# Optimization experiments

Measured on AMD Instinct MI355X. Metric: run time of the kernel, lower is better.

The kernel has to match this reference:

```python
import jax, jax.numpy as jnp
import numpy as np

EPS = 1e-8

def setup_inputs() -> dict:
    key = jax.random.key(0)
    ks = jax.random.split(key, 7)
    B, S, H, NH, V = 4, 2048, 1024, 8, 2048
    sc = 1.0 / np.sqrt(H)
    return {
        "hidden": jax.random.normal(ks[0], (B, S, H), jnp.float32),
        "prior_w": jax.random.normal(ks[1], (H, NH), jnp.float32) * sc,
        "prior_b": jnp.zeros((NH,), jnp.float32),
        "latent_w": jax.random.normal(ks[2], (H, NH * H), jnp.float32) * sc,
        "latent_b": jnp.zeros((NH * H,), jnp.float32),
        "output_w": jax.random.normal(ks[3], (H, V), jnp.float32) * sc,
        "output_b": jnp.zeros((V,), jnp.float32),
    }

def reference(hidden, prior_w, prior_b, latent_w, latent_b, output_w, output_b):
    B, S, H = hidden.shape
    NH = prior_w.shape[1]
    # prior: sigmoid then renormalize over heads
    prior = jax.nn.sigmoid(hidden @ prior_w + prior_b)              # [B,S,NH]
    prior = prior / (prior.sum(-1, keepdims=True) + EPS)
    # latent: linear -> [B,S,NH,H] -> tanh
    latent = jnp.tanh((hidden @ latent_w + latent_b).reshape(B, S, NH, H))
    # per-head softmax over vocab, weighted sum over heads
    logits = jnp.einsum('bsnh,hv->bsnv', latent, output_w) + output_b
    probs = jax.nn.softmax(logits, axis=-1)                          # [B,S,NH,V]
    return jnp.einsum('bsn,bsnv->bsv', prior, probs)
```

## Files before the change

### kernel.cpp

```cpp
#include <hip/hip_runtime.h>
#include <hip/hip_bf16.h>
#include <stdint.h>

typedef _Float16 f16;
typedef _Float16 f16x8 __attribute__((ext_vector_type(8)));
typedef _Float16 f16x4 __attribute__((ext_vector_type(4)));
typedef float f32x4 __attribute__((ext_vector_type(4)));
typedef float f32x16 __attribute__((ext_vector_type(16)));

#define T_TOK 8192
#define H_DIM 1024
#define NHEAD 8
#define V_DIM 2048

__device__ __forceinline__ void gload16(const void* g, void* l) {
  __builtin_amdgcn_global_load_lds(
      (const __attribute__((address_space(1))) void*)(uintptr_t)g,
      (__attribute__((address_space(3))) void*)(unsigned)(uintptr_t)l,
      16, 0, 0);
}

__device__ __forceinline__ float fast_tanh(float x) {
  float xc = fminf(fmaxf(x, -12.f), 12.f);
  float e = __expf(2.f * xc);
  return (e - 1.f) / (e + 1.f);
}

__device__ __forceinline__ void stage_half(const f16* __restrict__ gRowBase,
                                           char* ldsHalf, int tid, int sl8,
                                           int Kd) {
  const int srow = tid >> 3;
  char* wuni = ldsHalf + ((tid >> 6) << 10);
  gload16(gRowBase + (size_t)srow * Kd + sl8, wuni);
  gload16(gRowBase + (size_t)(srow + 64) * Kd + sl8, wuni + 8192);
}

template <int TANH, int NMAJ>
__global__ __launch_bounds__(512, 2) void k_gemm(const f16* __restrict__ A,
                                                 const f16* __restrict__ Bt,
                                                 const float* __restrict__ bias,
                                                 f16* __restrict__ C,
                                                 int M, int N, int K) {
  __shared__ __align__(16) f16 sA[2][16384];
  __shared__ __align__(16) f16 sB[2][16384];
  const int tid = threadIdx.x;
  const int lane = tid & 63;
  const int wid = tid >> 6;
  const int wr = wid >> 2, wc = wid & 3;
  const int gx = gridDim.x, gy = gridDim.y;
  const int id = blockIdx.y * gx + blockIdx.x;
  const int cpx = (gx * gy) >> 3;
  const int sw = (id & 7) * cpx + (id >> 3);
  int m0, n0;
  if (NMAJ) {
    n0 = (sw / gy) * 256;
    m0 = (sw % gy) * 256;
  } else {
    m0 = (sw / gx) * 256;
    n0 = (sw % gx) * 256;
  }
  const int NT = K >> 6;
  const int sl8 = ((tid & 7) ^ ((tid >> 3) & 7)) << 3;
  const int rr31 = lane & 31;
  const int hi = lane >> 5;
  const int l7 = lane & 7;

  const f16* Ag = A + (size_t)m0 * K;
  const f16* Bg = Bt + (size_t)n0 * K;
  char* sAb = (char*)&sA[0][0];
  char* sBb = (char*)&sB[0][0];

  stage_half(Ag, sAb, tid, sl8, K);
  stage_half(Ag + (size_t)128 * K, sAb + 16384, tid, sl8, K);
  stage_half(Bg, sBb, tid, sl8, K);
  stage_half(Bg + (size_t)128 * K, sBb + 16384, tid, sl8, K);
  stage_half(Bg + 64, sBb + 32768, tid, sl8, K);
  stage_half(Bg + (size_t)128 * K + 64, sBb + 32768 + 16384, tid, sl8, K);
  asm volatile("s_waitcnt vmcnt(4)" ::: "memory");
  __builtin_amdgcn_s_barrier();
  __builtin_amdgcn_sched_barrier(0);

  f32x16 acc[4][2] = {};
  f16x8 af0[4], af1[4], bf[2][4];

#define LDA_SET(dst, base, q)                                                  \
  {                                                                            \
    _Pragma("unroll") for (int mi = 0; mi < 4; ++mi) {                         \
      dst[mi] = *(const f16x8*)((base) + wr * 16384 + mi * 4096 + rr31 * 128 + \
                                (((2 * (q) + hi) ^ l7) << 4));                 \
    }                                                                          \
  }
#define LDB(base)                                                              \
  {                                                                            \
    _Pragma("unroll") for (int n = 0; n < 2; ++n) {                            \
      _Pragma("unroll") for (int ks = 0; ks < 4; ++ks) {                       \
        bf[n][ks] = *(const f16x8*)((base) + wc * 8192 + n * 4096 +            \
                                    rr31 * 128 + (((2 * ks + hi) ^ l7) << 4)); \
      }                                                                        \
    }                                                                          \
  }
#define MFMA8(ks, S)                                                           \
  {                                                                            \
    __builtin_amdgcn_s_setprio(1);                                             \
    _Pragma("unroll") for (int mi = 0; mi < 4; ++mi) {                         \
      _Pragma("unroll") for (int n = 0; n < 2; ++n) {                          \
        acc[mi][n] = __builtin_amdgcn_mfma_f32_32x32x16_f16(                   \
            S[mi], bf[n][ks], acc[mi][n], 0, 0, 0);                            \
      }                                                                        \
    }                                                                          \
    __builtin_amdgcn_s_setprio(0);                                             \
  }

  LDA_SET(af0, sAb, 0);

#define HALF(tt, bc)                                                           \
  {                                                                            \
    const char* cA = sAb + (bc)*32768;                                         \
    const char* cB = sBb + (bc)*32768;                                         \
    char* nA = sAb + ((bc) ^ 1) * 32768;                                       \
    char* nB = sBb + (bc)*32768;                                               \
    const int ktA = ((tt) + 1) << 6, ktB = ((tt) + 2) << 6;                    \
    const bool doA = (tt) + 1 < NT, doB = (tt) + 2 < NT;                       \
                                                                      \
    if (doA) stage_half(Ag + ktA, nA, tid, sl8, K);                            \
    LDB(cB);                                                                   \
    LDA_SET(af1, cA, 1);                                                       \
    __builtin_amdgcn_sched_barrier(0);                                         \
    MFMA8(0, af0);                                                             \
    __builtin_amdgcn_s_barrier();                                              \
                                                                      \
    if (doA) stage_half(Ag + (size_t)128 * K + ktA, nA + 16384, tid, sl8, K);  \
    LDA_SET(af0, cA, 2);                                                       \
    __builtin_amdgcn_sched_barrier(0);                                         \
    MFMA8(1, af1);                                                             \
    __builtin_amdgcn_s_barrier();                                              \
                                                                      \
    if (doB) stage_half(Bg + ktB, nB, tid, sl8, K);                            \
    LDA_SET(af1, cA, 3);                                                       \
    __builtin_amdgcn_sched_barrier(0);                                         \
    MFMA8(2, af0);                                                             \
    __builtin_amdgcn_s_barrier();                                              \
                  \
    if (doB) stage_half(Bg + (size_t)128 * K + ktB, nB + 16384, tid, sl8, K);  \
    if (doB) {                                                                 \
      asm volatile("s_waitcnt vmcnt(4)" ::: "memory");                         \
    } else {                                                                   \
      asm volatile("s_waitcnt vmcnt(0)" ::: "memory");                         \
    }                                                                          \
    __builtin_amdgcn_s_barrier();                                              \
    __builtin_amdgcn_sched_barrier(0);                                         \
    if (doA) LDA_SET(af0, sAb + ((bc) ^ 1) * 32768, 0);                        \
    __builtin_amdgcn_sched_barrier(0);                                         \
    MFMA8(3, af1);                                                             \
  }

#pragma unroll 1
  for (int T = 0; T < NT; T += 2) {
    HALF(T, 0);
    HALF(T + 1, 1);
  }
#undef HALF
#undef LDA_SET
#undef LDB
#undef MFMA8

  const int ccol0 = n0 + wc * 64 + rr31;
  float bv[2];
#pragma unroll
  for (int n = 0; n < 2; ++n) bv[n] = bias[ccol0 + n * 32];
#pragma unroll
  for (int mi = 0; mi < 4; ++mi) {
#pragma unroll
    for (int rq = 0; rq < 4; ++rq) {
#pragma unroll
      for (int r2 = 0; r2 < 4; ++r2) {
        const int row = m0 + wr * 128 + mi * 32 + r2 + 8 * rq + 4 * hi;
        f16* Crow = C + (size_t)row * N;
#pragma unroll
        for (int n = 0; n < 2; ++n) {
          float v = acc[mi][n][rq * 4 + r2] + bv[n];
          if (TANH) v = fast_tanh(v);
          Crow[ccol0 + n * 32] = (f16)v;
        }
      }
    }
  }
}

__global__ __launch_bounds__(256) void k_convert(const float* __restrict__ in,
                                                 f16* __restrict__ out, int n4) {
  int i = blockIdx.x * blockDim.x + threadIdx.x;
  if (i >= n4) return;
  const float4 v = ((const float4*)in)[i];
  f16x4 o;
  o[0] = (f16)v.x; o[1] = (f16)v.y; o[2] = (f16)v.z; o[3] = (f16)v.w;
  ((f16x4*)out)[i] = o;
}

__global__ __launch_bounds__(256) void k_transpose(const float* __restrict__ in,
                                                   f16* __restrict__ out,
                                                   int R, int C) {
  __shared__ f16 tile[64][66];
  const int c0 = blockIdx.x * 64, r0 = blockIdx.y * 64;
  const int tid = threadIdx.x;
  const int tr = tid >> 4;
  const int tc4 = (tid & 15) * 4;
#pragma unroll
  for (int i = 0; i < 4; ++i) {
    const int r = tr + i * 16;
    const float4 v = *(const float4*)&in[(size_t)(r0 + r) * C + c0 + tc4];
    tile[tc4 + 0][r] = (f16)v.x;
    tile[tc4 + 1][r] = (f16)v.y;
    tile[tc4 + 2][r] = (f16)v.z;
    tile[tc4 + 3][r] = (f16)v.w;
  }
  __syncthreads();
  const int oc = tid >> 2;
  const int or4 = (tid & 3) * 16;
#pragma unroll
  for (int i = 0; i < 4; ++i) {
    f16x4 w;
    w[0] = tile[oc][or4 + i * 4 + 0];
    w[1] = tile[oc][or4 + i * 4 + 1];
    w[2] = tile[oc][or4 + i * 4 + 2];
    w[3] = tile[oc][or4 + i * 4 + 3];
    *(f16x4*)&out[(size_t)(c0 + oc) * R + r0 + or4 + i * 4] = w;
  }
}

__global__ __launch_bounds__(256) void k_prior(const float* __restrict__ hidden,
                                               const float* __restrict__ pw,
                                               const float* __restrict__ pb,
                                               float* __restrict__ prior) {
  const int wid = threadIdx.x >> 6, lane = threadIdx.x & 63;
  const int t = blockIdx.x * 4 + wid;
  float acc[NHEAD] = {0.f, 0.f, 0.f, 0.f, 0.f, 0.f, 0.f, 0.f};
  const float* hrow = hidden + (size_t)t * H_DIM;
  for (int k = lane; k < H_DIM; k += 64) {
    float x = hrow[k];
    const float* wr = pw + k * NHEAD;
#pragma unroll
    for (int h = 0; h < NHEAD; ++h) acc[h] += x * wr[h];
  }
#pragma unroll
  for (int h = 0; h < NHEAD; ++h) {
#pragma unroll
    for (int off = 32; off >= 1; off >>= 1) acc[h] += __shfl_xor(acc[h], off);
  }
  if (lane == 0) {
    float p[NHEAD], s = 0.f;
#pragma unroll
    for (int h = 0; h < NHEAD; ++h) {
      p[h] = 1.f / (1.f + __expf(-(acc[h] + pb[h])));
      s += p[h];
    }
    float inv = 1.f / (s + 1e-8f);
#pragma unroll
    for (int h = 0; h < NHEAD; ++h) prior[t * NHEAD + h] = p[h] * inv;
  }
}

__global__ __launch_bounds__(256) void k_softmax(const f16* __restrict__ logits,
                                                 const float* __restrict__ prior,
                                                 float* __restrict__ out) {
  __shared__ float redsm[NHEAD * 4];
  const int t = blockIdx.x;
  const int tid = threadIdx.x, lane = tid & 63, wid = tid >> 6;
  const f16* base = logits + (size_t)t * NHEAD * V_DIM + tid * 8;

  f16x8 x[NHEAD];
#pragma unroll
  for (int h = 0; h < NHEAD; ++h) x[h] = *(const f16x8*)(base + h * V_DIM);

  float xv[NHEAD][8];
  float sml[NHEAD];
#pragma unroll
  for (int h = 0; h < NHEAD; ++h) {
    float s = 0.f;
#pragma unroll
    for (int j = 0; j < 8; ++j) {
      xv[h][j] = __expf(fminf((float)x[h][j], 50.f));
      s += xv[h][j];
    }
    sml[h] = s;
  }
#pragma unroll
  for (int h = 0; h < NHEAD; ++h) {
#pragma unroll
    for (int off = 32; off >= 1; off >>= 1) sml[h] += __shfl_xor(sml[h], off);
  }
  if (lane == 0) {
#pragma unroll
    for (int h = 0; h < NHEAD; ++h) redsm[h * 4 + wid] = sml[h];
  }
  __syncthreads();

  float oa[8] = {0.f, 0.f, 0.f, 0.f, 0.f, 0.f, 0.f, 0.f};
#pragma unroll
  for (int h = 0; h < NHEAD; ++h) {
    const float s = redsm[h * 4 + 0] + redsm[h * 4 + 1] + redsm[h * 4 + 2] +
                    redsm[h * 4 + 3];
    const float coef = prior[t * NHEAD + h] / s;
#pragma unroll
    for (int j = 0; j < 8; ++j) oa[j] += coef * xv[h][j];
  }
  float4* op = (float4*)(out + (size_t)t * V_DIM + tid * 8);
  op[0] = make_float4(oa[0], oa[1], oa[2], oa[3]);
  op[1] = make_float4(oa[4], oa[5], oa[6], oa[7]);
}

extern "C" void kernel_launch(void* const* d_in, const int* in_sizes, int n_in,
                              void* d_out, int out_size, void* d_ws, size_t ws_size,
                              hipStream_t stream) {
  const float* hidden   = (const float*)d_in[0];
  const float* prior_w  = (const float*)d_in[1];
  const float* prior_b  = (const float*)d_in[2];
  const float* latent_w = (const float*)d_in[3];
  const float* latent_b = (const float*)d_in[4];
  const float* output_w = (const float*)d_in[5];
  const float* output_b = (const float*)d_in[6];
  float* out = (float*)d_out;

  char* ws = (char*)d_ws;
  size_t off = 0;
  auto alloc = [&](size_t bytes) -> void* {
    void* p = ws + off;
    off += (bytes + 255) & ~(size_t)255;
    return p;
  };
  f16* hidden_h = (f16*)alloc((size_t)T_TOK * H_DIM * 2);
  f16* lw_t     = (f16*)alloc((size_t)NHEAD * H_DIM * H_DIM * 2);
  f16* ow_t     = (f16*)alloc((size_t)V_DIM * H_DIM * 2);
  float* prior  = (float*)alloc((size_t)T_TOK * NHEAD * 4);

  int tc = T_TOK;
  while (tc > 256) {
    size_t need = off + (size_t)tc * NHEAD * H_DIM * 2 + 256 +
                  (size_t)tc * NHEAD * V_DIM * 2 + 256;
    if (need <= ws_size) break;
    tc >>= 1;
  }
  f16* latent_h = (f16*)alloc((size_t)tc * NHEAD * H_DIM * 2);
  f16* logits_h = (f16*)alloc((size_t)tc * NHEAD * V_DIM * 2);

  k_convert<<<(T_TOK * H_DIM / 4 + 255) / 256, 256, 0, stream>>>(
      hidden, hidden_h, T_TOK * H_DIM / 4);
  k_transpose<<<dim3(NHEAD * H_DIM / 64, H_DIM / 64), 256, 0, stream>>>(
      latent_w, lw_t, H_DIM, NHEAD * H_DIM);
  k_transpose<<<dim3(V_DIM / 64, H_DIM / 64), 256, 0, stream>>>(
      output_w, ow_t, H_DIM, V_DIM);
  k_prior<<<T_TOK / 4, 256, 0, stream>>>(hidden, prior_w, prior_b, prior);

  const int nchunk = T_TOK / tc;
  for (int c = 0; c < nchunk; ++c) {
    const f16* Ah = hidden_h + (size_t)c * tc * H_DIM;
    k_gemm<1, 1><<<dim3(NHEAD * H_DIM / 256, tc / 256), 512, 0, stream>>>(
        Ah, lw_t, latent_b, latent_h, tc, NHEAD * H_DIM, H_DIM);
    k_gemm<0, 0><<<dim3(V_DIM / 256, tc * NHEAD / 256), 512, 0, stream>>>(
        latent_h, ow_t, output_b, logits_h, tc * NHEAD, V_DIM, H_DIM);
    k_softmax<<<tc, 256, 0, stream>>>(logits_h, prior + (size_t)c * tc * NHEAD,
                                      out + (size_t)c * tc * V_DIM);
  }
}
```

Measured before the change: 572.6 us.

## Fuse hidden conversion into prior kernel, rework softmax per-wave, split logits GEMM

The fp16 conversion of hidden is merged into the prior kernel so hidden is read once instead of twice. The softmax kernel now gives each wavefront one token: heads are processed one at a time with the next head's loads prefetched, and the shared-memory reduction and block barrier are gone. The logits GEMM is split into two half-M launches, which adds a launch and changes grid shape without reducing work. The softmax rewrite trades block-level parallelism for fewer synchronizations and higher per-thread register use.

Result: slower. 599.1 us (+4.6%).

```diff
diff --git a/kernel.cpp b/kernel.cpp
--- a/kernel.cpp
+++ b/kernel.cpp
@@ -187,16 +187,6 @@
   }
 }
 
-__global__ __launch_bounds__(256) void k_convert(const float* __restrict__ in,
-                                                 f16* __restrict__ out, int n4) {
-  int i = blockIdx.x * blockDim.x + threadIdx.x;
-  if (i >= n4) return;
-  const float4 v = ((const float4*)in)[i];
-  f16x4 o;
-  o[0] = (f16)v.x; o[1] = (f16)v.y; o[2] = (f16)v.z; o[3] = (f16)v.w;
-  ((f16x4*)out)[i] = o;
-}
-
 __global__ __launch_bounds__(256) void k_transpose(const float* __restrict__ in,
                                                    f16* __restrict__ out,
                                                    int R, int C) {
@@ -228,19 +218,30 @@
   }
 }
 
-__global__ __launch_bounds__(256) void k_prior(const float* __restrict__ hidden,
-                                               const float* __restrict__ pw,
-                                               const float* __restrict__ pb,
-                                               float* __restrict__ prior) {
+__global__ __launch_bounds__(256) void k_prior_conv(const float* __restrict__ hidden,
+                                                    const float* __restrict__ pw,
+                                                    const float* __restrict__ pb,
+                                                    float* __restrict__ prior,
+                                                    f16* __restrict__ hidden_h) {
   const int wid = threadIdx.x >> 6, lane = threadIdx.x & 63;
   const int t = blockIdx.x * 4 + wid;
+  const float* hrow = hidden + (size_t)t * H_DIM;
+  f16* orow = hidden_h + (size_t)t * H_DIM;
   float acc[NHEAD] = {0.f, 0.f, 0.f, 0.f, 0.f, 0.f, 0.f, 0.f};
-  const float* hrow = hidden + (size_t)t * H_DIM;
-  for (int k = lane; k < H_DIM; k += 64) {
-    float x = hrow[k];
-    const float* wr = pw + k * NHEAD;
-#pragma unroll
-    for (int h = 0; h < NHEAD; ++h) acc[h] += x * wr[h];
+#pragma unroll
+  for (int i = 0; i < 4; ++i) {
+    const int k = i * 256 + lane * 4;
+    const float4 v = *(const float4*)(hrow + k);
+    f16x4 o;
+    o[0] = (f16)v.x; o[1] = (f16)v.y; o[2] = (f16)v.z; o[3] = (f16)v.w;
+    *(f16x4*)(orow + k) = o;
+    const float vv[4] = {v.x, v.y, v.z, v.w};
+#pragma unroll
+    for (int j = 0; j < 4; ++j) {
+      const float* wr = pw + (size_t)(k + j) * NHEAD;
+#pragma unroll
+      for (int h = 0; h < NHEAD; ++h) acc[h] += vv[j] * wr[h];
+    }
   }
 #pragma unroll
   for (int h = 0; h < NHEAD; ++h) {
@@ -263,50 +264,52 @@
 __global__ __launch_bounds__(256) void k_softmax(const f16* __restrict__ logits,
                                                  const float* __restrict__ prior,
                                                  float* __restrict__ out) {
-  __shared__ float redsm[NHEAD * 4];
-  const int t = blockIdx.x;
-  const int tid = threadIdx.x, lane = tid & 63, wid = tid >> 6;
-  const f16* base = logits + (size_t)t * NHEAD * V_DIM + tid * 8;
-
-  f16x8 x[NHEAD];
-#pragma unroll
-  for (int h = 0; h < NHEAD; ++h) x[h] = *(const f16x8*)(base + h * V_DIM);
-
-  float xv[NHEAD][8];
-  float sml[NHEAD];
-#pragma unroll
+  const int wid = threadIdx.x >> 6, lane = threadIdx.x & 63;
+  const int t = blockIdx.x * 4 + wid;
+  const f16* base = logits + (size_t)t * NHEAD * V_DIM + lane * 32;
+
+  float oa[32];
+#pragma unroll
+  for (int j = 0; j < 32; ++j) oa[j] = 0.f;
+
+  f16x8 cx0 = *(const f16x8*)(base + 0);
+  f16x8 cx1 = *(const f16x8*)(base + 8);
+  f16x8 cx2 = *(const f16x8*)(base + 16);
+  f16x8 cx3 = *(const f16x8*)(base + 24);
+
+#pragma unroll 1
   for (int h = 0; h < NHEAD; ++h) {
+    const int hn = (h < NHEAD - 1) ? h + 1 : h;
+    const f16* nb = base + (size_t)hn * V_DIM;
+    f16x8 nx0 = *(const f16x8*)(nb + 0);
+    f16x8 nx1 = *(const f16x8*)(nb + 8);
+    f16x8 nx2 = *(const f16x8*)(nb + 16);
+    f16x8 nx3 = *(const f16x8*)(nb + 24);
+
+    float e[32];
     float s = 0.f;
 #pragma unroll
-    for (int j = 0; j < 8; ++j) {
-      xv[h][j] = __expf(fminf((float)x[h][j], 50.f));
-      s += xv[h][j];
-    }
-    sml[h] = s;
-  }
-#pragma unroll
-  for (int h = 0; h < NHEAD; ++h) {
-#pragma unroll
-    for (int off = 32; off >= 1; off >>= 1) sml[h] += __shfl_xor(sml[h], off);
-  }
-  if (lane == 0) {
-#pragma unroll
-    for (int h = 0; h < NHEAD; ++h) redsm[h * 4 + wid] = sml[h];
-  }
-  __syncthreads();
-
-  float oa[8] = {0.f, 0.f, 0.f, 0.f, 0.f, 0.f, 0.f, 0.f};
-#pragma unroll
-  for (int h = 0; h < NHEAD; ++h) {
-    const float s = redsm[h * 4 + 0] + redsm[h * 4 + 1] + redsm[h * 4 + 2] +
-                    redsm[h * 4 + 3];
+    for (int j = 0; j < 8; ++j) e[j] = __expf(fminf((float)cx0[j], 50.f));
+#pragma unroll
+    for (int j = 0; j < 8; ++j) e[8 + j] = __expf(fminf((float)cx1[j], 50.f));
+#pragma unroll
+    for (int j = 0; j < 8; ++j) e[16 + j] = __expf(fminf((float)cx2[j], 50.f));
+#pragma unroll
+    for (int j = 0; j < 8; ++j) e[24 + j] = __expf(fminf((float)cx3[j], 50.f));
+#pragma unroll
+    for (int j = 0; j < 32; ++j) s += e[j];
+#pragma unroll
+    for (int off = 32; off >= 1; off >>= 1) s += __shfl_xor(s, off);
     const float coef = prior[t * NHEAD + h] / s;
 #pragma unroll
-    for (int j = 0; j < 8; ++j) oa[j] += coef * xv[h][j];
-  }
-  float4* op = (float4*)(out + (size_t)t * V_DIM + tid * 8);
-  op[0] = make_float4(oa[0], oa[1], oa[2], oa[3]);
-  op[1] = make_float4(oa[4], oa[5], oa[6], oa[7]);
+    for (int j = 0; j < 32; ++j) oa[j] += coef * e[j];
+    cx0 = nx0; cx1 = nx1; cx2 = nx2; cx3 = nx3;
+  }
+
+  float4* op = (float4*)(out + (size_t)t * V_DIM + lane * 32);
+#pragma unroll
+  for (int j = 0; j < 8; ++j)
+    op[j] = make_float4(oa[4 * j], oa[4 * j + 1], oa[4 * j + 2], oa[4 * j + 3]);
 }
 
 extern "C" void kernel_launch(void* const* d_in, const int* in_sizes, int n_in,
@@ -343,22 +346,26 @@
   f16* latent_h = (f16*)alloc((size_t)tc * NHEAD * H_DIM * 2);
   f16* logits_h = (f16*)alloc((size_t)tc * NHEAD * V_DIM * 2);
 
-  k_convert<<<(T_TOK * H_DIM / 4 + 255) / 256, 256, 0, stream>>>(
-      hidden, hidden_h, T_TOK * H_DIM / 4);
+  k_prior_conv<<<T_TOK / 4, 256, 0, stream>>>(hidden, prior_w, prior_b, prior,
+                                              hidden_h);
   k_transpose<<<dim3(NHEAD * H_DIM / 64, H_DIM / 64), 256, 0, stream>>>(
       latent_w, lw_t, H_DIM, NHEAD * H_DIM);
   k_transpose<<<dim3(V_DIM / 64, H_DIM / 64), 256, 0, stream>>>(
       output_w, ow_t, H_DIM, V_DIM);
-  k_prior<<<T_TOK / 4, 256, 0, stream>>>(hidden, prior_w, prior_b, prior);
 
   const int nchunk = T_TOK / tc;
   for (int c = 0; c < nchunk; ++c) {
     const f16* Ah = hidden_h + (size_t)c * tc * H_DIM;
     k_gemm<1, 1><<<dim3(NHEAD * H_DIM / 256, tc / 256), 512, 0, stream>>>(
         Ah, lw_t, latent_b, latent_h, tc, NHEAD * H_DIM, H_DIM);
-    k_gemm<0, 0><<<dim3(V_DIM / 256, tc * NHEAD / 256), 512, 0, stream>>>(
-        latent_h, ow_t, output_b, logits_h, tc * NHEAD, V_DIM, H_DIM);
-    k_softmax<<<tc, 256, 0, stream>>>(logits_h, prior + (size_t)c * tc * NHEAD,
-                                      out + (size_t)c * tc * V_DIM);
-  }
-}
+    const int MH = tc * NHEAD / 2;
+    for (int s = 0; s < 2; ++s) {
+      k_gemm<0, 0><<<dim3(V_DIM / 256, MH / 256), 512, 0, stream>>>(
+          latent_h + (size_t)s * MH * H_DIM, ow_t, output_b,
+          logits_h + (size_t)s * MH * V_DIM, MH, V_DIM, H_DIM);
+    }
+    k_softmax<<<tc / 4, 256, 0, stream>>>(logits_h,
+                                          prior + (size_t)c * tc * NHEAD,
+                                          out + (size_t)c * tc * V_DIM);
+  }
+}
```
